# Kernel optimization log

Measured on AMD Instinct MI355X. Metric: run time of the kernel, lower is better.

The kernel has to match this reference:

```python
import jax, jax.numpy as jnp
import numpy as np

H, D = 8, 16            # num_heads, head_size
IN = H * D              # hgt_in_dim = 128
NT, ET = 3, 4           # node types, edge types (hard-coded in module)
N_DRUG, N_DIS, N_PROT = 10000, 10000, 30000
N = N_DRUG + N_DIS + N_PROT
E = 400000
LAYERS = 2
SQRT_D = float(np.sqrt(D))

# homogeneous node-type vector (presorted by type, as dgl.to_homogeneous yields)
NTYPE = jnp.concatenate([
    jnp.zeros(N_DRUG, jnp.int32),
    jnp.ones(N_DIS, jnp.int32),
    jnp.full((N_PROT,), 2, jnp.int32),
])


def typed_linear(x, types, W):
    # x: (M, in), W: (T, in, out), types: (M,) -> y[m] = x[m] @ W[types[m]]
    out = jnp.zeros((x.shape[0], W.shape[2]), x.dtype)
    for t in range(W.shape[0]):
        out = out + jnp.where((types == t)[:, None], x @ W[t], 0.0)
    return out


def hgt_conv(x, src, dst, etype, Wk, Wq, Wv, Wa, rel_att, rel_msg, pri, skip):
    # type-specific K/Q/V projections
    k = typed_linear(x, NTYPE, Wk).reshape(N, H, D)
    q = typed_linear(x, NTYPE, Wq).reshape(N, H, D)
    v = typed_linear(x, NTYPE, Wv).reshape(N, H, D)
    ke, qe, ve = k[src], q[dst], v[src]          # (E, H, D) gathers

    # per-edge-type relation transforms (vectorized over heads)
    kw = jnp.zeros_like(ke)
    mw = jnp.zeros_like(ve)
    for t in range(ET):
        sel = (etype == t)[:, None, None]
        kw = kw + jnp.where(sel, jnp.einsum('ehd,hdo->eho', ke, rel_att[:, t]), 0.0)
        mw = mw + jnp.where(sel, jnp.einsum('ehd,hdo->eho', ve, rel_msg[:, t]), 0.0)

    # attention logits: (kw . q) * relation_pri[head, etype] / sqrt(D)
    a = (kw * qe).sum(-1) * pri.T[etype] / SQRT_D  # (E, H)

    # edge softmax grouped by destination node, per head
    amax = jax.ops.segment_max(a, dst, num_segments=N)      # (N, H)
    ea = jnp.exp(a - amax[dst])
    esum = jax.ops.segment_sum(ea, dst, num_segments=N)
    attn = ea / esum[dst]                                   # (E, H)

    # weighted message aggregation (scatter-add over dst)
    m = mw * attn[..., None]                                 # (E, H, D)
    h = jax.ops.segment_sum(m, dst, num_segments=N).reshape(N, IN)

    # output projection (dropout = identity in eval) + sigmoid-skip residual
    h = typed_linear(h, NTYPE, Wa)
    alpha = jax.nn.sigmoid(skip)[NTYPE][:, None]
    return h * alpha + x * (1.0 - alpha)


def setup_inputs() -> dict:
    key = jax.random.key(0)
    ks = jax.random.split(key, 12)
    s = 0.05
    return {
        "drug_feature": jax.random.normal(ks[0], (N_DRUG, IN), jnp.float32),
        "disease_feature": jax.random.normal(ks[1], (N_DIS, IN), jnp.float32),
        "protein_feature": jax.random.normal(ks[2], (N_PROT, IN), jnp.float32),
        "src": jax.random.randint(ks[3], (E,), 0, N, dtype=jnp.int32),
        "dst": jax.random.randint(ks[4], (E,), 0, N, dtype=jnp.int32),
        "etype": jnp.sort(jax.random.randint(ks[5], (E,), 0, ET, dtype=jnp.int32)),
        "Wk": jax.random.normal(ks[6], (NT, IN, IN), jnp.float32) * s,
        "Wq": jax.random.normal(ks[7], (NT, IN, IN), jnp.float32) * s,
        "Wv": jax.random.normal(ks[8], (NT, IN, IN), jnp.float32) * s,
        "Wa": jax.random.normal(ks[9], (NT, IN, IN), jnp.float32) * s,
        "rel_att": jax.random.normal(ks[10], (H, ET, D, D), jnp.float32) * 0.1,
        "rel_msg": jax.random.normal(ks[11], (H, ET, D, D), jnp.float32) * 0.1,
        "pri": jnp.ones((H, ET), jnp.float32),
        "skip": jnp.ones((NT,), jnp.float32),
    }


def reference(drug_feature, disease_feature, protein_feature, src, dst, etype,
              Wk, Wq, Wv, Wa, rel_att, rel_msg, pri, skip):
    x = jnp.concatenate([drug_feature, disease_feature, protein_feature], axis=0)
    # ModuleList holds the SAME conv instance -> shared weights across layers
    for _ in range(LAYERS):
        x = hgt_conv(x, src, dst, etype, Wk, Wq, Wv, Wa, rel_att, rel_msg, pri, skip)
    return x
```

## Files before the change

kernel.cpp:

```cpp
#include <hip/hip_runtime.h>

#define N_NODE 50000
#define N_EDGE 400000
#define INF    128

#define FUSED_BLOCKS 1024
#define QA_BLOCKS    1024

#define MT0 157
#define MT1 157
#define MT2 469
#define MTILES 783

typedef __bf16 bf16x8 __attribute__((ext_vector_type(8)));
typedef float  f32x4  __attribute__((ext_vector_type(4)));

__device__ __forceinline__ void seg_decode64(int b, int& ty, int& base, int& nrows) {
  if (b < MT0)          { ty = 0; base = b * 64;                nrows = 10000 - base; }
  else if (b < MT0+MT1) { ty = 1; base = 10000 + (b - MT0)*64;  nrows = 20000 - base; }
  else                  { ty = 2; base = 20000 + (b-MT0-MT1)*64; nrows = 50000 - base; }
  if (nrows > 64) nrows = 64;
}

__device__ __forceinline__ float blo(unsigned u) { return __uint_as_float(u << 16); }
__device__ __forceinline__ float bhi(unsigned u) { return __uint_as_float(u & 0xffff0000u); }
__device__ __forceinline__ unsigned bpack(float lo, float hi) {
  unsigned a = __float_as_uint(lo), b = __float_as_uint(hi);
  a = (a + 0x7fffu + ((a >> 16) & 1u)) >> 16;
  b = (b + 0x7fffu + ((b >> 16) & 1u)) & 0xffff0000u;
  return a | b;
}
__device__ __forceinline__ unsigned short b16(float v) {
  unsigned u = __float_as_uint(v);
  return (unsigned short)((u + 0x7fffu + ((u >> 16) & 1u)) >> 16);
}
__device__ __forceinline__ bf16x8 ld_frag(const unsigned short* p) {
  uint4 u = *reinterpret_cast<const uint4*>(p);
  return __builtin_bit_cast(bf16x8, u);
}

__global__ __launch_bounds__(256) void k_concat(const float* __restrict__ dr,
                                                const float* __restrict__ di,
                                                const float* __restrict__ pr,
                                                float* __restrict__ x,
                                                unsigned short* __restrict__ xh) {
  for (int i = blockIdx.x * 256 + threadIdx.x; i < N_NODE * 32; i += 2048 * 256) {
    int row = i >> 5;
    float4 val;
    if (row < 10000)      val = ((const float4*)dr)[i];
    else if (row < 20000) val = ((const float4*)di)[i - 10000*32];
    else                  val = ((const float4*)pr)[i - 20000*32];
    ((float4*)x)[i] = val;
    ((uint2*)xh)[i] = make_uint2(bpack(val.x, val.y), bpack(val.z, val.w));
  }
}

__global__ __launch_bounds__(256) void k_count(const int* __restrict__ dst, int* __restrict__ deg) {
  int e = blockIdx.x * 256 + threadIdx.x;
  if (e < N_EDGE) atomicAdd(&deg[dst[e]], 1);
}

__global__ __launch_bounds__(1024) void k_scan(const int* __restrict__ deg,
                                               int* __restrict__ off, int* __restrict__ cur) {
  __shared__ int part[1024];
  int t = threadIdx.x;
  int c0 = t * 49;
  int c1 = c0 + 49; if (c1 > N_NODE) c1 = N_NODE;
  int s = 0;
  for (int i = c0; i < c1; ++i) s += deg[i];
  part[t] = s;
  __syncthreads();
  for (int ofs = 1; ofs < 1024; ofs <<= 1) {
    int v = (t >= ofs) ? part[t - ofs] : 0;
    __syncthreads();
    part[t] += v;
    __syncthreads();
  }
  int run = (t == 0) ? 0 : part[t - 1];
  for (int i = c0; i < c1; ++i) { off[i] = run; cur[i] = run; run += deg[i]; }
  if (t == 1023) off[N_NODE] = part[1023];
}

__global__ __launch_bounds__(256) void k_fill(const int* __restrict__ dst,
                                              const int* __restrict__ src,
                                              const int* __restrict__ etp,
                                              int* __restrict__ cur, int* __restrict__ est) {
  int e = blockIdx.x * 256 + threadIdx.x;
  if (e < N_EDGE) {
    int p = atomicAdd(&cur[dst[e]], 1);
    est[p] = (src[e] << 2) | etp[e];
  }
}

__global__ __launch_bounds__(256) void k_trmsg(const float* __restrict__ rm,
                                               float* __restrict__ AmT) {
  int i = blockIdx.x * 256 + threadIdx.x;
  int di = i & 15, doo = (i >> 4) & 15, ty = (i >> 8) & 3, hh = i >> 10;
  AmT[i] = rm[((hh * 4 + ty) * 16 + di) * 16 + doo];
}

__global__ __launch_bounds__(256) void k_twt(const float* __restrict__ Wk,
                                             const float* __restrict__ Wq,
                                             const float* __restrict__ Wv,
                                             const float* __restrict__ Wa,
                                             unsigned short* __restrict__ WT) {
  int idx = blockIdx.x * 256 + threadIdx.x;
  if (idx >= 196608) return;
  int mt = idx >> 14;
  int within = idx & 16383;
  int o = within >> 7, ii = within & 127;
  int mat = mt / 3, ty = mt % 3;
  const float* W = (mat == 0) ? Wk : (mat == 1) ? Wq : (mat == 2) ? Wv : Wa;
  WT[idx] = b16(W[ty * 16384 + ii * 128 + o]);
}

__global__ __launch_bounds__(256) void k_qkv(const unsigned short* __restrict__ xh,
                                             const unsigned short* __restrict__ WT,
                                             uint2* __restrict__ kvb,
                                             unsigned* __restrict__ qbh) {
  int ty, base, nrows;
  seg_decode64(blockIdx.x, ty, base, nrows);
  int w = threadIdx.x >> 6, l = threadIdx.x & 63;
  int r16 = l & 15, ks = l >> 4;
  int row0 = base + w * 16;
  int wrows = nrows - w * 16;

  bf16x8 a[4];
  const unsigned short* xrow = xh + (size_t)(row0 + r16) * 128 + ks * 8;
#pragma unroll
  for (int kk = 0; kk < 4; ++kk) a[kk] = ld_frag(xrow + kk * 32);

  const unsigned short* WK = WT + (size_t)(0 * 3 + ty) * 16384;
  const unsigned short* WQ = WT + (size_t)(1 * 3 + ty) * 16384;
  const unsigned short* WV = WT + (size_t)(2 * 3 + ty) * 16384;

#pragma unroll 1
  for (int ct = 0; ct < 8; ++ct) {
    int o = ct * 16 + r16;
    const unsigned short* bk = WK + (size_t)o * 128 + ks * 8;
    const unsigned short* bq = WQ + (size_t)o * 128 + ks * 8;
    const unsigned short* bv = WV + (size_t)o * 128 + ks * 8;
    f32x4 ak = {0.f,0.f,0.f,0.f}, aq = {0.f,0.f,0.f,0.f}, av = {0.f,0.f,0.f,0.f};
#pragma unroll
    for (int kk = 0; kk < 4; ++kk) {
      bf16x8 fbk = ld_frag(bk + kk * 32);
      bf16x8 fbq = ld_frag(bq + kk * 32);
      bf16x8 fbv = ld_frag(bv + kk * 32);
      ak = __builtin_amdgcn_mfma_f32_16x16x32_bf16(a[kk], fbk, ak, 0, 0, 0);
      aq = __builtin_amdgcn_mfma_f32_16x16x32_bf16(a[kk], fbq, aq, 0, 0, 0);
      av = __builtin_amdgcn_mfma_f32_16x16x32_bf16(a[kk], fbv, av, 0, 0, 0);
    }
#pragma unroll
    for (int r = 0; r < 4; ++r) {
      int rrel = ks * 4 + r;
      float kn = __shfl_xor(ak[r], 1);
      float qn = __shfl_xor(aq[r], 1);
      float vn = __shfl_xor(av[r], 1);
      if (rrel < wrows && (l & 1) == 0) {
        size_t p = (size_t)(row0 + rrel);
        kvb[p * 64 + (o >> 1)] = make_uint2(bpack(ak[r], kn), bpack(av[r], vn));
        qbh[p * 64 + (o >> 1)] = bpack(aq[r], qn);
      }
    }
  }
}

__global__ __launch_bounds__(256) void k_qa(const unsigned* __restrict__ qbh,
                                            const float* __restrict__ rel_att,
                                            const float* __restrict__ pri,
                                            uint4* __restrict__ qab) {
  int w = threadIdx.x >> 6, l = threadIdx.x & 63;
  int h = l >> 3, j = l & 7;
  float4 prh = ((const float4*)pri)[h];
  float prs[4] = { prh.x * 0.25f, prh.y * 0.25f, prh.z * 0.25f, prh.w * 0.25f };
  for (int n = blockIdx.x * 4 + w; n < N_NODE; n += QA_BLOCKS * 4) {
    const uint4* qp = (const uint4*)qbh + (size_t)n * 16 + h * 2;
    uint4 u0 = qp[0], u1 = qp[1];
    float qf[16];
    qf[0]=blo(u0.x); qf[1]=bhi(u0.x); qf[2]=blo(u0.y); qf[3]=bhi(u0.y);
    qf[4]=blo(u0.z); qf[5]=bhi(u0.z); qf[6]=blo(u0.w); qf[7]=bhi(u0.w);
    qf[8]=blo(u1.x); qf[9]=bhi(u1.x); qf[10]=blo(u1.y); qf[11]=bhi(u1.y);
    qf[12]=blo(u1.z); qf[13]=bhi(u1.z); qf[14]=blo(u1.w); qf[15]=bhi(u1.w);
    unsigned pk[4];
#pragma unroll
    for (int ty = 0; ty < 4; ++ty) {
      const float* Ar = rel_att + (((h * 4 + ty) * 16) + 2 * j) * 16;
      float ax = 0.f, ay = 0.f;
#pragma unroll
      for (int o = 0; o < 16; ++o) {
        ax += Ar[o] * qf[o];
        ay += Ar[16 + o] * qf[o];
      }
      pk[ty] = bpack(ax * prs[ty], ay * prs[ty]);
    }
    qab[(size_t)n * 64 + l] = make_uint4(pk[0], pk[1], pk[2], pk[3]);
  }
}

__global__ __launch_bounds__(256)
__attribute__((amdgpu_waves_per_eu(4, 4)))
void k_fused(const uint2* __restrict__ kvb,
             const uint4* __restrict__ qab,
             const int* __restrict__ off,
             const int* __restrict__ est,
             const float* __restrict__ AmT,
             unsigned* __restrict__ hbh) {
  __shared__ float accs[4][4][128];
  int w = threadIdx.x >> 6, l = threadIdx.x & 63;
  int h = l >> 3, j = l & 7;

  for (int n = blockIdx.x * 4 + w; n < N_NODE; n += FUSED_BLOCKS * 4) {
    int o0 = off[n], o1 = off[n + 1];

    uint4 qu = qab[(size_t)n * 64 + l];
    float2 qa0 = make_float2(blo(qu.x), bhi(qu.x));
    float2 qa1 = make_float2(blo(qu.y), bhi(qu.y));
    float2 qa2 = make_float2(blo(qu.z), bhi(qu.z));
    float2 qa3 = make_float2(blo(qu.w), bhi(qu.w));

    float ssum = 0.f;
    float2 z = make_float2(0.f, 0.f);
    float2 at0 = z, at1 = z, at2 = z, at3 = z;

#define PROC(KV, TY, VALID) { \
    int ty = (TY) & 3; \
    float kx = blo((KV).x), ky = bhi((KV).x); \
    float2 qat = (ty==0)?qa0:(ty==1)?qa1:(ty==2)?qa2:qa3; \
    float part = kx*qat.x + ky*qat.y; \
    part += __shfl_xor(part, 1); \
    part += __shfl_xor(part, 2); \
    part += __shfl_xor(part, 4); \
    float wgt = (VALID) ? __expf(part) : 0.f; \
    ssum += wgt; \
    float vx = blo((KV).y), vy = bhi((KV).y); \
    float w0=(ty==0)?wgt:0.f, w1=(ty==1)?wgt:0.f, w2=(ty==2)?wgt:0.f, w3=(ty==3)?wgt:0.f; \
    at0.x += w0*vx; at0.y += w0*vy; \
    at1.x += w1*vx; at1.y += w1*vy; \
    at2.x += w2*vx; at2.y += w2*vy; \
    at3.x += w3*vx; at3.y += w3*vy; }

    for (int b0 = o0; b0 < o1; b0 += 64) {
      int cnt = o1 - b0; if (cnt > 64) cnt = 64;
      int stv = est[b0 + l];
      int t0 = __shfl(stv, 0);
      int t1 = __shfl(stv, 1 < cnt ? 1 : 0);
      uint2 kv0 = kvb[(size_t)(t0 >> 2) * 64 + l];
      uint2 kv1 = kvb[(size_t)(t1 >> 2) * 64 + l];
      for (int i = 0; i < cnt; i += 2) {
        bool more = (i + 2) < cnt;
        int n0 = 0, n1 = 0; uint2 kn0, kn1;
        if (more) {
          n0 = __shfl(stv, i + 2);
          n1 = __shfl(stv, (i + 3) < cnt ? (i + 3) : (i + 2));
          kn0 = kvb[(size_t)(n0 >> 2) * 64 + l];
          kn1 = kvb[(size_t)(n1 >> 2) * 64 + l];
        }
        PROC(kv0, t0, true)
        PROC(kv1, t1, (i + 1) < cnt)
        if (more) { t0 = n0; t1 = n1; kv0 = kn0; kv1 = kn1; }
      }
    }
#undef PROC

    float inv = (ssum > 0.f) ? 1.f / ssum : 0.f;
    at0.x *= inv; at0.y *= inv;
    at1.x *= inv; at1.y *= inv;
    at2.x *= inv; at2.y *= inv;
    at3.x *= inv; at3.y *= inv;

    ((float2*)&accs[w][0][0])[l] = at0;
    ((float2*)&accs[w][1][0])[l] = at1;
    ((float2*)&accs[w][2][0])[l] = at2;
    ((float2*)&accs[w][3][0])[l] = at3;

    float ox = 0.f, oy = 0.f;
#pragma unroll
    for (int ty = 0; ty < 4; ++ty) {
      const float4* AmR = (const float4*)(AmT + ((h * 4 + ty) * 16) * 16);
#pragma unroll
      for (int d4 = 0; d4 < 4; ++d4) {
        float4 ac = *((float4*)&accs[w][ty][h * 16 + d4 * 4]);
        float4 m0 = AmR[(2 * j) * 4 + d4];
        float4 m1 = AmR[(2 * j + 1) * 4 + d4];
        ox += m0.x * ac.x + m0.y * ac.y + m0.z * ac.z + m0.w * ac.w;
        oy += m1.x * ac.x + m1.y * ac.y + m1.z * ac.z + m1.w * ac.w;
      }
    }
    hbh[(size_t)n * 64 + l] = bpack(ox, oy);
  }
}

__global__ __launch_bounds__(256) void k_out(const unsigned short* __restrict__ hbh,
                                             const unsigned short* __restrict__ WT,
                                             const float* __restrict__ skipv,
                                             float* __restrict__ xio,
                                             unsigned short* __restrict__ xh,
                                             int write_xh) {
  int ty, base, nrows;
  seg_decode64(blockIdx.x, ty, base, nrows);
  int w = threadIdx.x >> 6, l = threadIdx.x & 63;
  int r16 = l & 15, ks = l >> 4;
  int row0 = base + w * 16;
  int wrows = nrows - w * 16;

  bf16x8 a[4];
  const unsigned short* hrow = hbh + (size_t)(row0 + r16) * 128 + ks * 8;
#pragma unroll
  for (int kk = 0; kk < 4; ++kk) a[kk] = ld_frag(hrow + kk * 32);

  const unsigned short* WA = WT + (size_t)(3 * 3 + ty) * 16384;
  float alpha = 1.f / (1.f + __expf(-skipv[ty]));
  float beta = 1.f - alpha;

#pragma unroll 1
  for (int ct = 0; ct < 8; ++ct) {
    int o = ct * 16 + r16;
    const unsigned short* ba = WA + (size_t)o * 128 + ks * 8;
    f32x4 acc = {0.f,0.f,0.f,0.f};
#pragma unroll
    for (int kk = 0; kk < 4; ++kk)
      acc = __builtin_amdgcn_mfma_f32_16x16x32_bf16(a[kk], ld_frag(ba + kk * 32), acc, 0, 0, 0);
#pragma unroll
    for (int r = 0; r < 4; ++r) {
      int rrel = ks * 4 + r;
      size_t p = (size_t)(row0 + rrel) * 128 + o;
      float nx = 0.f;
      if (rrel < wrows) {
        nx = acc[r] * alpha + xio[p] * beta;
        xio[p] = nx;
      }
      float nxn = __shfl_xor(nx, 1);
      if (write_xh && rrel < wrows && (l & 1) == 0)
        ((unsigned*)xh)[p >> 1] = bpack(nx, nxn);
    }
  }
}

extern "C" void kernel_launch(void* const* d_in, const int* in_sizes, int n_in,
                              void* d_out, int out_size, void* d_ws, size_t ws_size,
                              hipStream_t stream) {
  const float* drug = (const float*)d_in[0];
  const float* dis  = (const float*)d_in[1];
  const float* prot = (const float*)d_in[2];
  const int* src    = (const int*)d_in[3];
  const int* dst    = (const int*)d_in[4];
  const int* etp    = (const int*)d_in[5];
  const float* Wk   = (const float*)d_in[6];
  const float* Wq   = (const float*)d_in[7];
  const float* Wv   = (const float*)d_in[8];
  const float* Wa   = (const float*)d_in[9];
  const float* rel_att = (const float*)d_in[10];
  const float* rel_msg = (const float*)d_in[11];
  const float* pri  = (const float*)d_in[12];
  const float* skip = (const float*)d_in[13];
  float* x = (float*)d_out;

  char* w = (char*)d_ws;
  uint2*          kvb = (uint2*)(w + 0);
  unsigned*       qbh = (unsigned*)(w + 25600000);
  unsigned*       hbh = (unsigned*)(w + 38400000);
  uint4*          qab = (uint4*)(w + 51200000);
  unsigned short* xh  = (unsigned short*)(w + 102400000);
  unsigned short* WT  = (unsigned short*)(w + 115200000);
  float*          AmT = (float*)(w + 115593216);
  int*            off = (int*)(w + 115625984);
  int*            est = (int*)(w + 115826048);
  int*            deg = (int*)(w + 38400000);
  int*            cur = (int*)(w + 38600064);

  k_concat<<<2048, 256, 0, stream>>>(drug, dis, prot, x, xh);

  (void)hipMemsetAsync(deg, 0, N_NODE * sizeof(int), stream);
  (void)hipMemsetAsync(est + N_EDGE, 0, 64 * sizeof(int), stream);
  k_count<<<(N_EDGE + 255) / 256, 256, 0, stream>>>(dst, deg);
  k_scan<<<1, 1024, 0, stream>>>(deg, off, cur);
  k_fill<<<(N_EDGE + 255) / 256, 256, 0, stream>>>(dst, src, etp, cur, est);

  k_trmsg<<<32, 256, 0, stream>>>(rel_msg, AmT);
  k_twt<<<768, 256, 0, stream>>>(Wk, Wq, Wv, Wa, WT);

  for (int layer = 0; layer < 2; ++layer) {
    k_qkv<<<MTILES, 256, 0, stream>>>(xh, WT, kvb, qbh);
    k_qa<<<QA_BLOCKS, 256, 0, stream>>>(qbh, rel_att, pri, qab);
    k_fused<<<FUSED_BLOCKS, 256, 0, stream>>>(kvb, qab, off, est, AmT, hbh);
    k_out<<<MTILES, 256, 0, stream>>>((const unsigned short*)hbh, WT, skip, x, xh,
                                      layer == 0 ? 1 : 0);
  }
}
```

Measured before the change: 848.2 us.

## Store K/V in FP8 and deepen edge-gather prefetch in fused attention

```diff
diff --git a/kernel.cpp b/kernel.cpp
--- a/kernel.cpp
+++ b/kernel.cpp
@@ -4,7 +4,7 @@
 #define N_EDGE 400000
 #define INF    128
 
-#define FUSED_BLOCKS 1024
+#define FUSED_BLOCKS 1536
 #define QA_BLOCKS    1024
 
 #define MT0 157
@@ -116,7 +116,7 @@
 
 __global__ __launch_bounds__(256) void k_qkv(const unsigned short* __restrict__ xh,
                                              const unsigned short* __restrict__ WT,
-                                             uint2* __restrict__ kvb,
+                                             unsigned* __restrict__ kv8,
                                              unsigned* __restrict__ qbh) {
   int ty, base, nrows;
   seg_decode64(blockIdx.x, ty, base, nrows);
@@ -158,7 +158,9 @@
       float vn = __shfl_xor(av[r], 1);
       if (rrel < wrows && (l & 1) == 0) {
         size_t p = (size_t)(row0 + rrel);
-        kvb[p * 64 + (o >> 1)] = make_uint2(bpack(ak[r], kn), bpack(av[r], vn));
+        int u = __builtin_amdgcn_cvt_pk_fp8_f32(ak[r], kn, 0, false);
+        u = __builtin_amdgcn_cvt_pk_fp8_f32(av[r], vn, u, true);
+        kv8[p * 64 + (o >> 1)] = (unsigned)u;
         qbh[p * 64 + (o >> 1)] = bpack(aq[r], qn);
       }
     }
@@ -198,8 +200,8 @@
 }
 
 __global__ __launch_bounds__(256)
-__attribute__((amdgpu_waves_per_eu(4, 4)))
-void k_fused(const uint2* __restrict__ kvb,
+__attribute__((amdgpu_waves_per_eu(6, 6)))
+void k_fused(const unsigned* __restrict__ kv8,
              const uint4* __restrict__ qab,
              const int* __restrict__ off,
              const int* __restrict__ est,
@@ -224,41 +226,53 @@
 
 #define PROC(KV, TY, VALID) { \
     int ty = (TY) & 3; \
-    float kx = blo((KV).x), ky = bhi((KV).x); \
+    auto kk = __builtin_amdgcn_cvt_pk_f32_fp8((int)(KV), false); \
+    auto vv = __builtin_amdgcn_cvt_pk_f32_fp8((int)(KV), true); \
     float2 qat = (ty==0)?qa0:(ty==1)?qa1:(ty==2)?qa2:qa3; \
-    float part = kx*qat.x + ky*qat.y; \
+    float part = kk[0]*qat.x + kk[1]*qat.y; \
     part += __shfl_xor(part, 1); \
     part += __shfl_xor(part, 2); \
     part += __shfl_xor(part, 4); \
     float wgt = (VALID) ? __expf(part) : 0.f; \
     ssum += wgt; \
-    float vx = blo((KV).y), vy = bhi((KV).y); \
     float w0=(ty==0)?wgt:0.f, w1=(ty==1)?wgt:0.f, w2=(ty==2)?wgt:0.f, w3=(ty==3)?wgt:0.f; \
-    at0.x += w0*vx; at0.y += w0*vy; \
-    at1.x += w1*vx; at1.y += w1*vy; \
-    at2.x += w2*vx; at2.y += w2*vy; \
-    at3.x += w3*vx; at3.y += w3*vy; }
+    at0.x += w0*vv[0]; at0.y += w0*vv[1]; \
+    at1.x += w1*vv[0]; at1.y += w1*vv[1]; \
+    at2.x += w2*vv[0]; at2.y += w2*vv[1]; \
+    at3.x += w3*vv[0]; at3.y += w3*vv[1]; }
 
     for (int b0 = o0; b0 < o1; b0 += 64) {
       int cnt = o1 - b0; if (cnt > 64) cnt = 64;
       int stv = est[b0 + l];
-      int t0 = __shfl(stv, 0);
-      int t1 = __shfl(stv, 1 < cnt ? 1 : 0);
-      uint2 kv0 = kvb[(size_t)(t0 >> 2) * 64 + l];
-      uint2 kv1 = kvb[(size_t)(t1 >> 2) * 64 + l];
-      for (int i = 0; i < cnt; i += 2) {
-        bool more = (i + 2) < cnt;
-        int n0 = 0, n1 = 0; uint2 kn0, kn1;
+#define SLOT(I) (((I) < cnt) ? (I) : (cnt - 1))
+      int t0 = __shfl(stv, SLOT(0)), t1 = __shfl(stv, SLOT(1));
+      int t2 = __shfl(stv, SLOT(2)), t3 = __shfl(stv, SLOT(3));
+      unsigned kv0 = kv8[(size_t)(t0 >> 2) * 64 + l];
+      unsigned kv1 = kv8[(size_t)(t1 >> 2) * 64 + l];
+      unsigned kv2 = kv8[(size_t)(t2 >> 2) * 64 + l];
+      unsigned kv3 = kv8[(size_t)(t3 >> 2) * 64 + l];
+      for (int i = 0; i < cnt; i += 4) {
+        bool more = (i + 4) < cnt;
+        int n0 = 0, n1 = 0, n2 = 0, n3 = 0;
+        unsigned kn0, kn1, kn2, kn3;
         if (more) {
-          n0 = __shfl(stv, i + 2);
-          n1 = __shfl(stv, (i + 3) < cnt ? (i + 3) : (i + 2));
-          kn0 = kvb[(size_t)(n0 >> 2) * 64 + l];
-          kn1 = kvb[(size_t)(n1 >> 2) * 64 + l];
+          n0 = __shfl(stv, i + 4);
+          n1 = __shfl(stv, SLOT(i + 5));
+          n2 = __shfl(stv, SLOT(i + 6));
+          n3 = __shfl(stv, SLOT(i + 7));
+          kn0 = kv8[(size_t)(n0 >> 2) * 64 + l];
+          kn1 = kv8[(size_t)(n1 >> 2) * 64 + l];
+          kn2 = kv8[(size_t)(n2 >> 2) * 64 + l];
+          kn3 = kv8[(size_t)(n3 >> 2) * 64 + l];
         }
         PROC(kv0, t0, true)
         PROC(kv1, t1, (i + 1) < cnt)
-        if (more) { t0 = n0; t1 = n1; kv0 = kn0; kv1 = kn1; }
+        PROC(kv2, t2, (i + 2) < cnt)
+        PROC(kv3, t3, (i + 3) < cnt)
+        if (more) { t0 = n0; t1 = n1; t2 = n2; t3 = n3;
+                    kv0 = kn0; kv1 = kn1; kv2 = kn2; kv3 = kn3; }
       }
+#undef SLOT
     }
 #undef PROC
 
@@ -356,7 +370,7 @@
   float* x = (float*)d_out;
 
   char* w = (char*)d_ws;
-  uint2*          kvb = (uint2*)(w + 0);
+  unsigned*       kv8 = (unsigned*)(w + 0);
   unsigned*       qbh = (unsigned*)(w + 25600000);
   unsigned*       hbh = (unsigned*)(w + 38400000);
   uint4*          qab = (uint4*)(w + 51200000);
@@ -380,9 +394,9 @@
   k_twt<<<768, 256, 0, stream>>>(Wk, Wq, Wv, Wa, WT);
 
   for (int layer = 0; layer < 2; ++layer) {
-    k_qkv<<<MTILES, 256, 0, stream>>>(xh, WT, kvb, qbh);
+    k_qkv<<<MTILES, 256, 0, stream>>>(xh, WT, kv8, qbh);
     k_qa<<<QA_BLOCKS, 256, 0, stream>>>(qbh, rel_att, pri, qab);
-    k_fused<<<FUSED_BLOCKS, 256, 0, stream>>>(kvb, qab, off, est, AmT, hbh);
+    k_fused<<<FUSED_BLOCKS, 256, 0, stream>>>(kv8, qab, off, est, AmT, hbh);
     k_out<<<MTILES, 256, 0, stream>>>((const unsigned short*)hbh, WT, skip, x, xh,
                                       layer == 0 ? 1 : 0);
   }
```

Result: slower. 1.340 ms (+58.0%).
